# Performance work log

Hardware: AMD Instinct MI355X
Metric: run time of the kernel (lower is better)

The kernel has to match this reference:

```python
import jax, jax.numpy as jnp
import numpy as np

B, S, H = 64, 512, 768   # n_blocks, seq_len, hidden
C, M = 50, 2000          # n_characters, n_mentions
T = B * S                # total_seq_len
NEG_INF = -jnp.inf


def setup_inputs() -> dict:
    key = jax.random.key(0)
    ks = jax.random.split(key, 16)
    story_embeddings = jax.random.normal(ks[0], (B, S, H), dtype=jnp.float32)

    # additive log masks: 0.0 = allowed token, -inf = blocked (matches softmax(score + mask))
    names_bin = jax.random.bernoulli(ks[1], 0.05, (C, S)).at[:, 0].set(True)  # every char has >=1 name token
    names_mask = jnp.where(names_bin, 0.0, NEG_INF).astype(jnp.float32)

    utt_bin = jax.random.bernoulli(ks[2], 0.02, (C, T))
    utt_bin = utt_bin.at[40:].set(False)  # chars 40..49 have no utterances -> nan_to_num path
    utterances_mask = jnp.where(utt_bin, 0.0, NEG_INF).astype(jnp.float32)

    men_bin = jax.random.bernoulli(ks[3], 0.01, (M, T)).at[:, 0].set(True)
    mentions_mask = jnp.where(men_bin, 0.0, NEG_INF).astype(jnp.float32)

    mention_character_ids = jax.random.randint(ks[4], (M,), 0, 45, dtype=jnp.int32)  # chars 45..49 mention-less

    def lin(k):
        return 0.02 * jax.random.normal(k, (H,), dtype=jnp.float32)

    return {
        "story_embeddings": story_embeddings,
        "names_mask": names_mask,
        "utterances_mask": utterances_mask,
        "mentions_mask": mentions_mask,
        "mention_character_ids": mention_character_ids,
        "w_name_tok": lin(ks[5]), "b_name_tok": jnp.float32(0.0),
        "w_name": lin(ks[6]), "b_name": jnp.float32(0.0),
        "w_men_tok": lin(ks[7]), "b_men_tok": jnp.float32(0.0),
        "w_men": lin(ks[8]), "b_men": jnp.float32(0.0),
        "w_utt": lin(ks[9]), "b_utt": jnp.float32(0.0),
        "w_comb": lin(ks[10]), "b_comb": jnp.float32(0.0),
    }


def reference(story_embeddings, names_mask, utterances_mask, mentions_mask,
              mention_character_ids, w_name_tok, b_name_tok, w_name, b_name,
              w_men_tok, b_men_tok, w_men, b_men, w_utt, b_utt, w_comb, b_comb):
    n_char = names_mask.shape[0]
    n_blocks, seqlen, hidden = story_embeddings.shape
    se_flat = story_embeddings.reshape(n_blocks * seqlen, hidden)  # [T,H]

    # ---- name representation ----
    nts = story_embeddings @ w_name_tok + b_name_tok                       # [B,S]
    n_attn = jax.nn.softmax(nts[None, :, :] + names_mask[:, None, :], axis=2)  # [C,B,S]
    names_emb = jnp.einsum('cbs,bsh->cbh', n_attn, story_embeddings)       # [C,B,H]
    n_score = names_emb @ w_name + b_name                                  # [C,B]
    name_e = jnp.einsum('cb,cbh->ch', jax.nn.softmax(n_score, axis=1), names_emb)

    # ---- mention representation (segment softmax over mentions per character) ----
    mts = se_flat @ w_men_tok + b_men_tok                                  # [T]
    m_attn = jax.nn.softmax(mentions_mask + mts[None, :], axis=1)          # [M,T]
    m_emb = m_attn @ se_flat                                               # [M,H]
    m_score = m_emb @ w_men + b_men                                        # [M]
    seg = mention_character_ids
    seg_max = jax.ops.segment_max(m_score, seg, num_segments=n_char)       # [C]
    ex = jnp.exp(m_score - seg_max[seg])                                   # [M]
    den = jax.ops.segment_sum(ex, seg, num_segments=n_char)                # [C]
    mw = ex / den[seg]                                                     # [M]
    mention_e = jax.ops.segment_sum(mw[:, None] * m_emb, seg, num_segments=n_char)  # [C,H]; empty chars -> 0

    # ---- utterance representation ----
    uts = se_flat @ w_utt + b_utt                                          # [T]
    u_attn = jnp.nan_to_num(jax.nn.softmax(utterances_mask + uts[None, :], axis=1), nan=0.0)
    utt_e = u_attn @ se_flat                                               # [C,H]

    # ---- combine ----
    emb = jnp.stack([name_e, mention_e, utt_e], axis=1)                    # [C,3,H]
    score = emb @ w_comb + b_comb                                          # [C,3]
    has_mention = jax.ops.segment_sum(jnp.ones_like(m_score), seg, num_segments=n_char) > 0
    has_utt = jnp.any(utterances_mask == 0, axis=1)
    zeros = jnp.zeros((n_char,), dtype=score.dtype)
    mask = jnp.stack([zeros,
                      jnp.where(has_mention, 0.0, NEG_INF := -jnp.inf),
                      jnp.where(has_utt, 0.0, -jnp.inf)], axis=1)          # [C,3]
    attn = jax.nn.softmax(score + mask, axis=1)
    return jnp.einsum('ck,ckh->ch', attn, emb)                             # [C,H]
```

## Files before the change

kernel.cpp:

```cpp
#include <hip/hip_runtime.h>
#include <cmath>

#define Bn 64
#define Sn 512
#define Hn 768
#define Cn 50
#define Mn 2000
#define Tn (Bn*Sn)
#define MCAP 1024
#define NP 128
#define TC 256
#define HT 128

__global__ __launch_bounds__(256) void k_proj(
    const float* __restrict__ se,
    const float* __restrict__ w_ntok, const float* __restrict__ b_ntok,
    const float* __restrict__ w_name,
    const float* __restrict__ w_mtok, const float* __restrict__ b_mtok,
    const float* __restrict__ w_men,
    const float* __restrict__ w_utt, const float* __restrict__ b_utt,
    const float* __restrict__ w_comb,
    float* __restrict__ nts, float* __restrict__ p_name,
    float* __restrict__ mts, float* __restrict__ p_men,
    float* __restrict__ uts, float* __restrict__ p_comb)
{
    int wave = threadIdx.x >> 6, lane = threadIdx.x & 63;
    int r = blockIdx.x * 4 + wave;
    const float4* se4 = (const float4*)(se + (size_t)r * Hn);
    const float4* w0 = (const float4*)w_ntok;
    const float4* w1 = (const float4*)w_name;
    const float4* w2 = (const float4*)w_mtok;
    const float4* w3 = (const float4*)w_men;
    const float4* w4 = (const float4*)w_utt;
    const float4* w5 = (const float4*)w_comb;
    float s0=0,s1=0,s2=0,s3=0,s4=0,s5=0;
#pragma unroll
    for (int k = 0; k < 3; k++) {
        int i = lane + 64*k;
        float4 v = se4[i];
        float4 a;
        a = w0[i]; s0 += v.x*a.x + v.y*a.y + v.z*a.z + v.w*a.w;
        a = w1[i]; s1 += v.x*a.x + v.y*a.y + v.z*a.z + v.w*a.w;
        a = w2[i]; s2 += v.x*a.x + v.y*a.y + v.z*a.z + v.w*a.w;
        a = w3[i]; s3 += v.x*a.x + v.y*a.y + v.z*a.z + v.w*a.w;
        a = w4[i]; s4 += v.x*a.x + v.y*a.y + v.z*a.z + v.w*a.w;
        a = w5[i]; s5 += v.x*a.x + v.y*a.y + v.z*a.z + v.w*a.w;
    }
#pragma unroll
    for (int off = 32; off >= 1; off >>= 1) {
        s0 += __shfl_xor(s0, off); s1 += __shfl_xor(s1, off);
        s2 += __shfl_xor(s2, off); s3 += __shfl_xor(s3, off);
        s4 += __shfl_xor(s4, off); s5 += __shfl_xor(s5, off);
    }
    if (lane == 0) {
        nts[r]    = s0 + b_ntok[0];
        p_name[r] = s1;
        mts[r]    = s2 + b_mtok[0];
        p_men[r]  = s3;
        uts[r]    = s4 + b_utt[0];
        p_comb[r] = s5;
    }
}

__global__ __launch_bounds__(256) void k_names(
    const float* __restrict__ nm_mask, const float* __restrict__ nts,
    const float* __restrict__ p_name, const float* __restrict__ p_comb,
    const float* __restrict__ b_name_p,
    float* __restrict__ n_score, float* __restrict__ sc_n,
    float* __restrict__ m1n, float* __restrict__ denn)
{
    int wave = threadIdx.x >> 6, lane = threadIdx.x & 63;
    int idx = blockIdx.x * 4 + wave;
    int c = idx >> 6, b = idx & 63;
    float v[8];
    float mx = -INFINITY;
#pragma unroll
    for (int k = 0; k < 8; k++) {
        int s = lane + 64*k;
        float val = nm_mask[c*Sn + s] + nts[b*Sn + s];
        v[k] = val;
        mx = fmaxf(mx, val);
    }
#pragma unroll
    for (int off = 32; off >= 1; off >>= 1) mx = fmaxf(mx, __shfl_xor(mx, off));
    float d = 0, sn = 0, sc = 0;
#pragma unroll
    for (int k = 0; k < 8; k++) {
        int s = lane + 64*k;
        int t = b*Sn + s;
        float e = __expf(v[k] - mx);
        d += e; sn += e * p_name[t]; sc += e * p_comb[t];
    }
#pragma unroll
    for (int off = 32; off >= 1; off >>= 1) {
        d += __shfl_xor(d, off); sn += __shfl_xor(sn, off); sc += __shfl_xor(sc, off);
    }
    if (lane == 0) {
        n_score[idx] = sn / d + b_name_p[0];
        sc_n[idx]    = sc / d;
        m1n[idx]     = mx;
        denn[idx]    = d;
    }
}

__global__ __launch_bounds__(256) void k_scan(
    const float* __restrict__ mmask, const float* __restrict__ mts,
    const float* __restrict__ p_men, const float* __restrict__ p_comb,
    const float* __restrict__ b_men_p,
    const float* __restrict__ umask, const float* __restrict__ uts,
    float* __restrict__ m_score, float* __restrict__ mcv, float* __restrict__ denm,
    int* __restrict__ midx, float* __restrict__ mwgt, int* __restrict__ mcnt,
    float* __restrict__ m1u, float* __restrict__ denu, float* __restrict__ sc2)
{
    int tid = threadIdx.x;
    int wv = tid >> 6, lane = tid & 63;
    bool isU = blockIdx.x >= Mn;
    int row = isU ? (blockIdx.x - Mn) : blockIdx.x;

    __shared__ int scnt;
    __shared__ int   sT[MCAP];
    __shared__ float sV[MCAP];
    __shared__ float sr1[4], sr2[4], sr3[4], sr4[4];
    if (tid == 0) scnt = 0;
    __syncthreads();

    const float4* row4  = (const float4*)((isU ? umask : mmask) + (size_t)row * Tn);
    const float4* vals4 = (const float4*)(isU ? uts : mts);

    for (int k = 0; k < Tn/4/256; k++) {
        int i = tid + k*256;
        float4 f = row4[i];
        float4 v = vals4[i];
        float fm[4] = {f.x, f.y, f.z, f.w};
        float vv[4] = {v.x, v.y, v.z, v.w};
#pragma unroll
        for (int j = 0; j < 4; j++) {
            bool act = (fm[j] == 0.0f);
            unsigned long long bm = __ballot(act);
            if (bm) {
                int tot = __popcll(bm);
                int pos = __popcll(bm & ((1ull << lane) - 1ull));
                int base;
                if (lane == 0) base = atomicAdd(&scnt, tot);
                base = __shfl(base, 0);
                int s = base + pos;
                if (act && s < MCAP) { sT[s] = i*4 + j; sV[s] = vv[j]; }
            }
        }
    }
    __syncthreads();
    int n = (scnt < MCAP) ? scnt : MCAP;

    float mx = -INFINITY;
    for (int i = tid; i < n; i += 256) mx = fmaxf(mx, sV[i]);
#pragma unroll
    for (int off = 32; off >= 1; off >>= 1) mx = fmaxf(mx, __shfl_xor(mx, off));
    if (lane == 0) sr1[wv] = mx;
    __syncthreads();
    mx = fmaxf(fmaxf(sr1[0], sr1[1]), fmaxf(sr1[2], sr1[3]));

    float d = 0, nm = 0, nc = 0;
    if (!isU) {
        int* gi = midx + (size_t)row * MCAP;
        float* gwp = mwgt + (size_t)row * MCAP;
        for (int i = tid; i < n; i += 256) {
            float e = __expf(sV[i] - mx);
            int t = sT[i];
            d += e; nm += e * p_men[t]; nc += e * p_comb[t];
            gi[i] = t; gwp[i] = e;
        }
    } else {
        for (int i = tid; i < n; i += 256) {
            float e = __expf(sV[i] - mx);
            d += e; nc += e * p_comb[sT[i]];
        }
    }
#pragma unroll
    for (int off = 32; off >= 1; off >>= 1) {
        d += __shfl_xor(d, off); nm += __shfl_xor(nm, off); nc += __shfl_xor(nc, off);
    }
    if (lane == 0) { sr2[wv] = d; sr3[wv] = nm; sr4[wv] = nc; }
    __syncthreads();
    if (tid == 0) {
        float dd = sr2[0]+sr2[1]+sr2[2]+sr2[3];
        float sm = sr3[0]+sr3[1]+sr3[2]+sr3[3];
        float sc = sr4[0]+sr4[1]+sr4[2]+sr4[3];
        if (!isU) {
            m_score[row] = sm/dd + b_men_p[0];
            mcv[row]     = sc/dd;
            denm[row]    = dd;
            mcnt[row]    = n;
        } else {
            m1u[row]  = mx;
            denu[row] = dd;
            sc2[row]  = (dd > 0.f) ? sc/dd : 0.f;
        }
    }
}

__global__ __launch_bounds__(256) void k_small(
    const float* __restrict__ n_score, const float* __restrict__ sc_n,
    const int* __restrict__ seg, const float* __restrict__ m_score, const float* __restrict__ mcv,
    float* __restrict__ bw, float* __restrict__ sc0,
    float* __restrict__ segmax, float* __restrict__ segden, float* __restrict__ sc1)
{
    int tid = threadIdx.x;
    if (blockIdx.x < Cn) {
        int c = blockIdx.x;
        if (tid < 64) {
            int lane = tid;
            int idx = c*Bn + lane;
            float v = n_score[idx];
            float mx = v;
#pragma unroll
            for (int off = 32; off >= 1; off >>= 1) mx = fmaxf(mx, __shfl_xor(mx, off));
            float e = __expf(v - mx);
            float d = e, s = e * sc_n[idx];
#pragma unroll
            for (int off = 32; off >= 1; off >>= 1) { d += __shfl_xor(d, off); s += __shfl_xor(s, off); }
            bw[idx] = e / d;
            if (lane == 0) sc0[c] = s / d;
        }
    } else {
        int c = blockIdx.x - Cn;
        float mx = -INFINITY;
        for (int m = tid; m < Mn; m += 256)
            if (seg[m] == c) mx = fmaxf(mx, m_score[m]);
        __shared__ float sm[256];
        sm[tid] = mx; __syncthreads();
        for (int s = 128; s > 0; s >>= 1) { if (tid < s) sm[tid] = fmaxf(sm[tid], sm[tid+s]); __syncthreads(); }
        mx = sm[0];
        float d = 0, s1 = 0;
        if (mx != -INFINITY) {
            for (int m = tid; m < Mn; m += 256)
                if (seg[m] == c) { float e = __expf(m_score[m] - mx); d += e; s1 += e * mcv[m]; }
        }
        __shared__ float sd[256], ss[256];
        sd[tid] = d; ss[tid] = s1; __syncthreads();
        for (int s = 128; s > 0; s >>= 1) { if (tid < s) { sd[tid] += sd[tid+s]; ss[tid] += ss[tid+s]; } __syncthreads(); }
        if (tid == 0) {
            segmax[c] = mx;
            segden[c] = sd[0];
            sc1[c]    = (sd[0] > 0.f) ? ss[0]/sd[0] : 0.f;
        }
    }
}

__device__ inline void combine_attn(float sc0v, float sc1v, float sc2v,
                                    float sdn, float dnu, float bc,
                                    float& a0, float& a1, float& a2)
{
    float s0 = sc0v + bc;
    bool hasm = sdn > 0.f, hasu = dnu > 0.f;
    float s1 = hasm ? sc1v + bc : -INFINITY;
    float s2 = hasu ? sc2v + bc : -INFINITY;
    float mx = fmaxf(s0, fmaxf(s1, s2));
    float e0 = __expf(s0 - mx);
    float e1 = hasm ? __expf(s1 - mx) : 0.f;
    float e2 = hasu ? __expf(s2 - mx) : 0.f;
    float dd = e0 + e1 + e2;
    a0 = e0/dd; a1 = e1/dd; a2 = e2/dd;
}

__global__ __launch_bounds__(256) void k_buildW(
    const float* __restrict__ nm_mask, const float* __restrict__ nts,
    const float* __restrict__ m1n, const float* __restrict__ denn,
    const float* __restrict__ bw,
    const float* __restrict__ umask, const float* __restrict__ uts,
    const float* __restrict__ m1u, const float* __restrict__ denu,
    const float* __restrict__ sc0, const float* __restrict__ sc1, const float* __restrict__ sc2,
    const float* __restrict__ segden, const float* __restrict__ b_comb_p,
    float* __restrict__ W)
{
    int c = blockIdx.y;
    float a0, a1, a2;
    combine_attn(sc0[c], sc1[c], sc2[c], segden[c], denu[c], b_comb_p[0], a0, a1, a2);
    int t0 = (blockIdx.x * 256 + threadIdx.x) * 4;
    int b = t0 >> 9;
    float4 um = *(const float4*)(umask + (size_t)c * Tn + t0);
    float cn = a0 * bw[c*Bn + b] / denn[c*Bn + b];
    float m1nc = m1n[c*Bn + b];
    float du = denu[c];
    float cu = (du > 0.f) ? a2 / du : 0.f;
    float m1uc = m1u[c];
    float umj[4] = {um.x, um.y, um.z, um.w};
    float rj[4];
#pragma unroll
    for (int j = 0; j < 4; j++) {
        int t = t0 + j;
        int s = t & (Sn-1);
        float w = 0.f;
        if (nm_mask[c*Sn + s] == 0.f) w += cn * __expf(nts[t] - m1nc);
        if (umj[j] == 0.f)            w += cu * __expf(uts[t] - m1uc);
        rj[j] = w;
    }
    *(float4*)(W + (size_t)c * Tn + t0) = make_float4(rj[0], rj[1], rj[2], rj[3]);
}

__global__ __launch_bounds__(64) void k_scatter_men(
    const int* __restrict__ midx, const float* __restrict__ mwgt, const int* __restrict__ mcnt,
    const int* __restrict__ seg,
    const float* __restrict__ m_score, const float* __restrict__ denm,
    const float* __restrict__ segmax, const float* __restrict__ segden,
    const float* __restrict__ sc0, const float* __restrict__ sc1, const float* __restrict__ sc2,
    const float* __restrict__ denu, const float* __restrict__ b_comb_p,
    float* __restrict__ W)
{
    int m = blockIdx.x, tid = threadIdx.x;
    int c = seg[m];
    float a0, a1, a2;
    combine_attn(sc0[c], sc1[c], sc2[c], segden[c], denu[c], b_comb_p[0], a0, a1, a2);
    float coef = a1 * __expf(m_score[m] - segmax[c]) / segden[c] / denm[m];
    int n = mcnt[m];
    const int* gi = midx + (size_t)m * MCAP;
    const float* gwp = mwgt + (size_t)m * MCAP;
    float* Wc = W + (size_t)c * Tn;
    for (int i = tid; i < n; i += 64)
        atomicAdd(&Wc[gi[i]], coef * gwp[i]);
}

__global__ __launch_bounds__(256) void k_out1(
    const float* __restrict__ W, const float* __restrict__ se, float* __restrict__ partial)
{
    int p = blockIdx.x;
    int h0 = blockIdx.y * HT;
    int tid = threadIdx.x;
    int x = tid & 31, y = tid >> 5;
    __shared__ float sW[56][64];
    __shared__ float sS[64][128];
    float4 acc[7];
#pragma unroll
    for (int i = 0; i < 7; i++) acc[i] = make_float4(0,0,0,0);
    for (int sub = 0; sub < 4; sub++) {
        int tbase = p*TC + sub*64;
        for (int i = tid; i < 896; i += 256) {
            int c = i >> 4, f = i & 15;
            float4 v = (c < Cn) ? *(const float4*)(W + (size_t)c * Tn + tbase + f*4)
                                : make_float4(0,0,0,0);
            *(float4*)&sW[c][f*4] = v;
        }
#pragma unroll
        for (int q = 0; q < 8; q++) {
            int idx = tid + q*256;
            int row = idx >> 5, col = idx & 31;
            *(float4*)&sS[row][col*4] =
                *(const float4*)(se + (size_t)(tbase + row) * Hn + h0 + col*4);
        }
        __syncthreads();
        for (int t = 0; t < 64; t++) {
            float4 v = *(const float4*)&sS[t][x*4];
#pragma unroll
            for (int cc = 0; cc < 7; cc++) {
                float w = sW[y*7 + cc][t];
                acc[cc].x += w*v.x; acc[cc].y += w*v.y;
                acc[cc].z += w*v.z; acc[cc].w += w*v.w;
            }
        }
        __syncthreads();
    }
#pragma unroll
    for (int cc = 0; cc < 7; cc++) {
        int c = y*7 + cc;
        if (c < Cn)
            *(float4*)(partial + ((size_t)p * Cn + c) * Hn + h0 + x*4) = acc[cc];
    }
}

__global__ __launch_bounds__(256) void k_out2(
    const float* __restrict__ partial, float* __restrict__ out)
{
    int cell = blockIdx.x * 256 + threadIdx.x;
    if (cell < Cn*Hn) {
        float s = 0.f;
#pragma unroll 8
        for (int p = 0; p < NP; p++)
            s += partial[(size_t)p * (Cn*Hn) + cell];
        out[cell] = s;
    }
}

extern "C" void kernel_launch(void* const* d_in, const int* in_sizes, int n_in,
                              void* d_out, int out_size, void* d_ws, size_t ws_size,
                              hipStream_t stream) {
    const float* se      = (const float*)d_in[0];
    const float* nm_mask = (const float*)d_in[1];
    const float* umask   = (const float*)d_in[2];
    const float* mmask   = (const float*)d_in[3];
    const int*   seg     = (const int*)  d_in[4];
    const float* w_ntok  = (const float*)d_in[5];
    const float* b_ntok  = (const float*)d_in[6];
    const float* w_name  = (const float*)d_in[7];
    const float* b_name  = (const float*)d_in[8];
    const float* w_mtok  = (const float*)d_in[9];
    const float* b_mtok  = (const float*)d_in[10];
    const float* w_men   = (const float*)d_in[11];
    const float* b_men   = (const float*)d_in[12];
    const float* w_utt   = (const float*)d_in[13];
    const float* b_utt   = (const float*)d_in[14];
    const float* w_comb  = (const float*)d_in[15];
    const float* b_comb  = (const float*)d_in[16];
    float* out = (float*)d_out;

    float* ws = (float*)d_ws;
    float* partial = ws;
    float* W       = partial + (size_t)NP*Cn*Hn;
    float* nts     = W + (size_t)Cn*Tn;
    float* p_name  = nts + Tn;
    float* mts     = p_name + Tn;
    float* p_men   = mts + Tn;
    float* uts     = p_men + Tn;
    float* p_comb  = uts + Tn;
    float* n_score = p_comb + Tn;
    float* sc_n    = n_score + Cn*Bn;
    float* bw      = sc_n + Cn*Bn;
    float* m1n     = bw + Cn*Bn;
    float* denn    = m1n + Cn*Bn;
    float* m_score = denn + Cn*Bn;
    float* mcv     = m_score + Mn;
    float* denm    = mcv + Mn;
    float* mwgt    = denm + Mn;
    int*   midx    = (int*)(mwgt + (size_t)Mn*MCAP);
    int*   mcnt    = midx + (size_t)Mn*MCAP;
    float* segmax  = (float*)(mcnt + Mn);
    float* segden  = segmax + Cn;
    float* sc0     = segden + Cn;
    float* sc1     = sc0 + Cn;
    float* sc2     = sc1 + Cn;
    float* m1u     = sc2 + Cn;
    float* denu    = m1u + Cn;

    k_proj<<<Tn/4, 256, 0, stream>>>(se, w_ntok, b_ntok, w_name, w_mtok, b_mtok,
                                     w_men, w_utt, b_utt, w_comb,
                                     nts, p_name, mts, p_men, uts, p_comb);

    k_names<<<(Cn*Bn)/4, 256, 0, stream>>>(nm_mask, nts, p_name, p_comb, b_name,
                                           n_score, sc_n, m1n, denn);

    k_scan<<<Mn + Cn, 256, 0, stream>>>(mmask, mts, p_men, p_comb, b_men,
                                        umask, uts,
                                        m_score, mcv, denm, midx, mwgt, mcnt,
                                        m1u, denu, sc2);

    k_small<<<2*Cn, 256, 0, stream>>>(n_score, sc_n, seg, m_score, mcv,
                                      bw, sc0, segmax, segden, sc1);

    k_buildW<<<dim3(Tn/1024, Cn), 256, 0, stream>>>(nm_mask, nts, m1n, denn, bw,
                                                    umask, uts, m1u, denu,
                                                    sc0, sc1, sc2, segden, b_comb, W);

    k_scatter_men<<<Mn, 64, 0, stream>>>(midx, mwgt, mcnt, seg, m_score, denm,
                                         segmax, segden, sc0, sc1, sc2, denu, b_comb, W);

    k_out1<<<dim3(NP, Hn/HT), 256, 0, stream>>>(W, se, partial);
    k_out2<<<(Cn*Hn + 255)/256, 256, 0, stream>>>(partial, out);
}
```

Measured before the change: 195.0 us.

## Fuse names softmax into scan kernel, cache proj weights, vectorize out1 inner loop

After: 188.4 us. 1.03x faster.

```diff
diff --git a/kernel.cpp b/kernel.cpp
--- a/kernel.cpp
+++ b/kernel.cpp
@@ -24,82 +24,45 @@
     float* __restrict__ mts, float* __restrict__ p_men,
     float* __restrict__ uts, float* __restrict__ p_comb)
 {
-    int wave = threadIdx.x >> 6, lane = threadIdx.x & 63;
-    int r = blockIdx.x * 4 + wave;
-    const float4* se4 = (const float4*)(se + (size_t)r * Hn);
-    const float4* w0 = (const float4*)w_ntok;
-    const float4* w1 = (const float4*)w_name;
-    const float4* w2 = (const float4*)w_mtok;
-    const float4* w3 = (const float4*)w_men;
-    const float4* w4 = (const float4*)w_utt;
-    const float4* w5 = (const float4*)w_comb;
-    float s0=0,s1=0,s2=0,s3=0,s4=0,s5=0;
-#pragma unroll
-    for (int k = 0; k < 3; k++) {
-        int i = lane + 64*k;
-        float4 v = se4[i];
-        float4 a;
-        a = w0[i]; s0 += v.x*a.x + v.y*a.y + v.z*a.z + v.w*a.w;
-        a = w1[i]; s1 += v.x*a.x + v.y*a.y + v.z*a.z + v.w*a.w;
-        a = w2[i]; s2 += v.x*a.x + v.y*a.y + v.z*a.z + v.w*a.w;
-        a = w3[i]; s3 += v.x*a.x + v.y*a.y + v.z*a.z + v.w*a.w;
-        a = w4[i]; s4 += v.x*a.x + v.y*a.y + v.z*a.z + v.w*a.w;
-        a = w5[i]; s5 += v.x*a.x + v.y*a.y + v.z*a.z + v.w*a.w;
-    }
-#pragma unroll
-    for (int off = 32; off >= 1; off >>= 1) {
-        s0 += __shfl_xor(s0, off); s1 += __shfl_xor(s1, off);
-        s2 += __shfl_xor(s2, off); s3 += __shfl_xor(s3, off);
-        s4 += __shfl_xor(s4, off); s5 += __shfl_xor(s5, off);
-    }
-    if (lane == 0) {
-        nts[r]    = s0 + b_ntok[0];
-        p_name[r] = s1;
-        mts[r]    = s2 + b_mtok[0];
-        p_men[r]  = s3;
-        uts[r]    = s4 + b_utt[0];
-        p_comb[r] = s5;
-    }
-}
-
-__global__ __launch_bounds__(256) void k_names(
-    const float* __restrict__ nm_mask, const float* __restrict__ nts,
-    const float* __restrict__ p_name, const float* __restrict__ p_comb,
-    const float* __restrict__ b_name_p,
-    float* __restrict__ n_score, float* __restrict__ sc_n,
-    float* __restrict__ m1n, float* __restrict__ denn)
-{
-    int wave = threadIdx.x >> 6, lane = threadIdx.x & 63;
-    int idx = blockIdx.x * 4 + wave;
-    int c = idx >> 6, b = idx & 63;
-    float v[8];
-    float mx = -INFINITY;
-#pragma unroll
-    for (int k = 0; k < 8; k++) {
-        int s = lane + 64*k;
-        float val = nm_mask[c*Sn + s] + nts[b*Sn + s];
-        v[k] = val;
-        mx = fmaxf(mx, val);
-    }
-#pragma unroll
-    for (int off = 32; off >= 1; off >>= 1) mx = fmaxf(mx, __shfl_xor(mx, off));
-    float d = 0, sn = 0, sc = 0;
-#pragma unroll
-    for (int k = 0; k < 8; k++) {
-        int s = lane + 64*k;
-        int t = b*Sn + s;
-        float e = __expf(v[k] - mx);
-        d += e; sn += e * p_name[t]; sc += e * p_comb[t];
-    }
-#pragma unroll
-    for (int off = 32; off >= 1; off >>= 1) {
-        d += __shfl_xor(d, off); sn += __shfl_xor(sn, off); sc += __shfl_xor(sc, off);
-    }
-    if (lane == 0) {
-        n_score[idx] = sn / d + b_name_p[0];
-        sc_n[idx]    = sc / d;
-        m1n[idx]     = mx;
-        denn[idx]    = d;
+    int wv = threadIdx.x >> 6, lane = threadIdx.x & 63;
+    int gw = blockIdx.x * 4 + wv;
+    float4 w[6][3];
+    const float4* warr[6] = {(const float4*)w_ntok, (const float4*)w_name,
+                             (const float4*)w_mtok, (const float4*)w_men,
+                             (const float4*)w_utt,  (const float4*)w_comb};
+#pragma unroll
+    for (int j = 0; j < 6; j++)
+#pragma unroll
+        for (int k = 0; k < 3; k++) w[j][k] = warr[j][lane + 64*k];
+    float b0 = b_ntok[0], b2 = b_mtok[0], b4 = b_utt[0];
+    for (int rr = 0; rr < 8; rr++) {
+        int r = gw*8 + rr;
+        const float4* se4 = (const float4*)(se + (size_t)r * Hn);
+        float s0=0,s1=0,s2=0,s3=0,s4=0,s5=0;
+#pragma unroll
+        for (int k = 0; k < 3; k++) {
+            float4 v = se4[lane + 64*k];
+            s0 += v.x*w[0][k].x + v.y*w[0][k].y + v.z*w[0][k].z + v.w*w[0][k].w;
+            s1 += v.x*w[1][k].x + v.y*w[1][k].y + v.z*w[1][k].z + v.w*w[1][k].w;
+            s2 += v.x*w[2][k].x + v.y*w[2][k].y + v.z*w[2][k].z + v.w*w[2][k].w;
+            s3 += v.x*w[3][k].x + v.y*w[3][k].y + v.z*w[3][k].z + v.w*w[3][k].w;
+            s4 += v.x*w[4][k].x + v.y*w[4][k].y + v.z*w[4][k].z + v.w*w[4][k].w;
+            s5 += v.x*w[5][k].x + v.y*w[5][k].y + v.z*w[5][k].z + v.w*w[5][k].w;
+        }
+#pragma unroll
+        for (int off = 32; off >= 1; off >>= 1) {
+            s0 += __shfl_xor(s0, off); s1 += __shfl_xor(s1, off);
+            s2 += __shfl_xor(s2, off); s3 += __shfl_xor(s3, off);
+            s4 += __shfl_xor(s4, off); s5 += __shfl_xor(s5, off);
+        }
+        if (lane == 0) {
+            nts[r]    = s0 + b0;
+            p_name[r] = s1;
+            mts[r]    = s2 + b2;
+            p_men[r]  = s3;
+            uts[r]    = s4 + b4;
+            p_comb[r] = s5;
+        }
     }
 }
 
@@ -108,31 +71,69 @@
     const float* __restrict__ p_men, const float* __restrict__ p_comb,
     const float* __restrict__ b_men_p,
     const float* __restrict__ umask, const float* __restrict__ uts,
+    const float* __restrict__ nm_mask, const float* __restrict__ nts,
+    const float* __restrict__ p_name, const float* __restrict__ b_name_p,
     float* __restrict__ m_score, float* __restrict__ mcv, float* __restrict__ denm,
     int* __restrict__ midx, float* __restrict__ mwgt, int* __restrict__ mcnt,
-    float* __restrict__ m1u, float* __restrict__ denu, float* __restrict__ sc2)
+    float* __restrict__ m1u, float* __restrict__ denu, float* __restrict__ sc2,
+    float* __restrict__ n_score, float* __restrict__ sc_n,
+    float* __restrict__ m1n, float* __restrict__ denn)
 {
     int tid = threadIdx.x;
     int wv = tid >> 6, lane = tid & 63;
-    bool isU = blockIdx.x >= Mn;
-    int row = isU ? (blockIdx.x - Mn) : blockIdx.x;
 
     __shared__ int scnt;
     __shared__ int   sT[MCAP];
     __shared__ float sV[MCAP];
     __shared__ float sr1[4], sr2[4], sr3[4], sr4[4];
+
+    if (blockIdx.x >= Mn + Cn) {
+        int idx = (blockIdx.x - Mn - Cn) * 4 + wv;
+        int c = idx >> 6, b = idx & 63;
+        float v[8];
+        float mx = -INFINITY;
+#pragma unroll
+        for (int k = 0; k < 8; k++) {
+            int s = lane + 64*k;
+            float val = nm_mask[c*Sn + s] + nts[b*Sn + s];
+            v[k] = val;
+            mx = fmaxf(mx, val);
+        }
+#pragma unroll
+        for (int off = 32; off >= 1; off >>= 1) mx = fmaxf(mx, __shfl_xor(mx, off));
+        float d = 0, sn = 0, sc = 0;
+#pragma unroll
+        for (int k = 0; k < 8; k++) {
+            int s = lane + 64*k;
+            int t = b*Sn + s;
+            float e = __expf(v[k] - mx);
+            d += e; sn += e * p_name[t]; sc += e * p_comb[t];
+        }
+#pragma unroll
+        for (int off = 32; off >= 1; off >>= 1) {
+            d += __shfl_xor(d, off); sn += __shfl_xor(sn, off); sc += __shfl_xor(sc, off);
+        }
+        if (lane == 0) {
+            n_score[idx] = sn / d + b_name_p[0];
+            sc_n[idx]    = sc / d;
+            m1n[idx]     = mx;
+            denn[idx]    = d;
+        }
+        return;
+    }
+
+    bool isU = blockIdx.x >= Mn;
+    int row = isU ? (blockIdx.x - Mn) : blockIdx.x;
     if (tid == 0) scnt = 0;
     __syncthreads();
 
-    const float4* row4  = (const float4*)((isU ? umask : mmask) + (size_t)row * Tn);
-    const float4* vals4 = (const float4*)(isU ? uts : mts);
+    const float4* row4 = (const float4*)((isU ? umask : mmask) + (size_t)row * Tn);
+    const float*  vals = isU ? uts : mts;
 
     for (int k = 0; k < Tn/4/256; k++) {
         int i = tid + k*256;
         float4 f = row4[i];
-        float4 v = vals4[i];
         float fm[4] = {f.x, f.y, f.z, f.w};
-        float vv[4] = {v.x, v.y, v.z, v.w};
 #pragma unroll
         for (int j = 0; j < 4; j++) {
             bool act = (fm[j] == 0.0f);
@@ -142,9 +143,9 @@
                 int pos = __popcll(bm & ((1ull << lane) - 1ull));
                 int base;
                 if (lane == 0) base = atomicAdd(&scnt, tot);
-                base = __shfl(base, 0);
+                base = __builtin_amdgcn_readfirstlane(base);
                 int s = base + pos;
-                if (act && s < MCAP) { sT[s] = i*4 + j; sV[s] = vv[j]; }
+                if (act && s < MCAP) sT[s] = i*4 + j;
             }
         }
     }
@@ -152,7 +153,11 @@
     int n = (scnt < MCAP) ? scnt : MCAP;
 
     float mx = -INFINITY;
-    for (int i = tid; i < n; i += 256) mx = fmaxf(mx, sV[i]);
+    for (int i = tid; i < n; i += 256) {
+        float v = vals[sT[i]];
+        sV[i] = v;
+        mx = fmaxf(mx, v);
+    }
 #pragma unroll
     for (int off = 32; off >= 1; off >>= 1) mx = fmaxf(mx, __shfl_xor(mx, off));
     if (lane == 0) sr1[wv] = mx;
@@ -319,6 +324,7 @@
         atomicAdd(&Wc[gi[i]], coef * gwp[i]);
 }
 
+#define FMA4(A, WS, V) { A.x += (WS)*(V).x; A.y += (WS)*(V).y; A.z += (WS)*(V).z; A.w += (WS)*(V).w; }
 __global__ __launch_bounds__(256) void k_out1(
     const float* __restrict__ W, const float* __restrict__ se, float* __restrict__ partial)
 {
@@ -347,13 +353,21 @@
                 *(const float4*)(se + (size_t)(tbase + row) * Hn + h0 + col*4);
         }
         __syncthreads();
-        for (int t = 0; t < 64; t++) {
-            float4 v = *(const float4*)&sS[t][x*4];
+        for (int t4 = 0; t4 < 64; t4 += 4) {
+            float4 wq[7];
+#pragma unroll
+            for (int cc = 0; cc < 7; cc++)
+                wq[cc] = *(const float4*)&sW[y*7 + cc][t4];
+            float4 v0 = *(const float4*)&sS[t4+0][x*4];
+            float4 v1 = *(const float4*)&sS[t4+1][x*4];
+            float4 v2 = *(const float4*)&sS[t4+2][x*4];
+            float4 v3 = *(const float4*)&sS[t4+3][x*4];
 #pragma unroll
             for (int cc = 0; cc < 7; cc++) {
-                float w = sW[y*7 + cc][t];
-                acc[cc].x += w*v.x; acc[cc].y += w*v.y;
-                acc[cc].z += w*v.z; acc[cc].w += w*v.w;
+                FMA4(acc[cc], wq[cc].x, v0);
+                FMA4(acc[cc], wq[cc].y, v1);
+                FMA4(acc[cc], wq[cc].z, v2);
+                FMA4(acc[cc], wq[cc].w, v3);
             }
         }
         __syncthreads();
@@ -429,17 +443,17 @@
     float* m1u     = sc2 + Cn;
     float* denu    = m1u + Cn;
 
-    k_proj<<<Tn/4, 256, 0, stream>>>(se, w_ntok, b_ntok, w_name, w_mtok, b_mtok,
+    k_proj<<<1024, 256, 0, stream>>>(se, w_ntok, b_ntok, w_name, w_mtok, b_mtok,
                                      w_men, w_utt, b_utt, w_comb,
                                      nts, p_name, mts, p_men, uts, p_comb);
 
-    k_names<<<(Cn*Bn)/4, 256, 0, stream>>>(nm_mask, nts, p_name, p_comb, b_name,
-                                           n_score, sc_n, m1n, denn);
-
-    k_scan<<<Mn + Cn, 256, 0, stream>>>(mmask, mts, p_men, p_comb, b_men,
-                                        umask, uts,
-                                        m_score, mcv, denm, midx, mwgt, mcnt,
-                                        m1u, denu, sc2);
+    k_scan<<<Mn + Cn + (Cn*Bn)/4, 256, 0, stream>>>(
+        mmask, mts, p_men, p_comb, b_men,
+        umask, uts,
+        nm_mask, nts, p_name, b_name,
+        m_score, mcv, denm, midx, mwgt, mcnt,
+        m1u, denu, sc2,
+        n_score, sc_n, m1n, denn);
 
     k_small<<<2*Cn, 256, 0, stream>>>(n_score, sc_n, seg, m_score, mcv,
                                       bw, sc0, segmax, segden, sc1);
```
